# Kernel optimization log

Hardware: AMD Instinct MI355X
Metric: run time of the kernel (lower is better)

Reference implementation:

```python
import jax, jax.numpy as jnp
import numpy as np
from jax import lax

H = 1024   # hidden_size
C = 64     # cond_size
L = 256    # latent_size
V = 32000  # num_of_word
NC = 8     # num_of_cond
T = 256    # MAX_LENGTH == seq len (teacher forcing, full length)


def setup_inputs() -> dict:
    key = jax.random.key(0)
    ks = jax.random.split(key, 26)
    p = lambda k, shape, s=0.05: (jax.random.normal(k, shape, jnp.float32) * s)
    inp = {
        # learned parameters
        "cond_emb": p(ks[0], (NC, C)),
        "enc_emb": p(ks[1], (V, H)),
        "enc_wih": p(ks[2], (4 * H, H)), "enc_whh": p(ks[3], (4 * H, H)),
        "enc_bih": p(ks[4], (4 * H,)), "enc_bhh": p(ks[5], (4 * H,)),
        "mean_w": p(ks[6], (L, H)), "mean_b": p(ks[7], (L,)),
        "lgv_w": p(ks[8], (L, H)), "lgv_b": p(ks[9], (L,)),
        "l2h_w": p(ks[10], (H, L + C)), "l2h_b": p(ks[11], (H,)),
        "l2c_w": p(ks[12], (H, L + C)), "l2c_b": p(ks[13], (H,)),
        "dec_emb": p(ks[14], (V, H)),
        "dec_wih": p(ks[15], (4 * H, H)), "dec_whh": p(ks[16], (4 * H, H)),
        "dec_bih": p(ks[17], (4 * H,)), "dec_bhh": p(ks[18], (4 * H,)),
        "out_w": p(ks[19], (V, H)), "out_b": p(ks[20], (V,)),
        # reparameterization noise (torch.normal in sample_z)
        "eps": jax.random.normal(ks[21], (L,), jnp.float32),
        # forward args
        "input_ids": jax.random.randint(ks[22], (T,), 0, V),
        "target_ids": jax.random.randint(ks[23], (T,), 0, V),
        "input_c": 2,
        "target_c": 3,
    }
    return inp


def _lstm_cell(h, c, x, wih, whh, bih, bhh):
    # torch LSTM gate order: i, f, g, o
    g = x @ wih.T + bih + h @ whh.T + bhh
    i, f, gg, o = jnp.split(g, 4)
    c = jax.nn.sigmoid(f) * c + jax.nn.sigmoid(i) * jnp.tanh(gg)
    h = jax.nn.sigmoid(o) * jnp.tanh(c)
    return h, c


def reference(cond_emb, enc_emb, enc_wih, enc_whh, enc_bih, enc_bhh,
              mean_w, mean_b, lgv_w, lgv_b, l2h_w, l2h_b, l2c_w, l2c_b,
              dec_emb, dec_wih, dec_whh, dec_bih, dec_bhh, out_w, out_b,
              eps, input_ids, target_ids, input_c, target_c):
    Hd = enc_whh.shape[1]
    cond_in = cond_emb[input_c]                              # (C,)
    # encoder initial hidden = cat(zeros(H-C), cond); cell = zeros(H)
    h0 = jnp.concatenate([jnp.zeros(Hd - cond_in.shape[0], cond_in.dtype), cond_in])
    c0 = jnp.zeros(Hd, cond_in.dtype)
    enc_x = enc_emb[input_ids]                               # (T, H)

    def enc_step(carry, x):
        h, c = _lstm_cell(carry[0], carry[1], x, enc_wih, enc_whh, enc_bih, enc_bhh)
        return (h, c), None
    (hT, _), _ = lax.scan(enc_step, (h0, c0), enc_x)

    m = mean_w @ hT + mean_b                                 # (L,)
    lgv = lgv_w @ hT + lgv_b                                 # (L,)
    z = eps * jnp.exp(lgv / 2) + m                           # reparameterize

    zc = jnp.concatenate([z, cond_emb[target_c]])            # (L+C,)
    dh0 = l2h_w @ zc + l2h_b
    dc0 = l2c_w @ zc + l2c_b

    # teacher forcing: decoder inputs = [SOS=0, target[:-1]], T steps
    dec_in = jnp.concatenate([jnp.zeros((1,), target_ids.dtype), target_ids[:-1]])
    dec_x = dec_emb[dec_in]                                  # (T, H)

    def dec_step(carry, x):
        h, c = _lstm_cell(carry[0], carry[1], x, dec_wih, dec_whh, dec_bih, dec_bhh)
        return (h, c), h
    _, hs = lax.scan(dec_step, (dh0, dc0), dec_x)            # (T, H)

    logits = hs @ out_w.T + out_b                            # (T, V)
    return logits, m, lgv
```

## Files before the change

kernel.cpp:

```cpp
#include <hip/hip_runtime.h>
#include <hip/hip_bf16.h>

#define HD   1024
#define G4   4096
#define CND  64
#define LAT  256
#define VOC  32000
#define TT   256
#define ZCN  320
#define NWG  128
#define DEC0 301u

typedef unsigned long long u64;
typedef __attribute__((ext_vector_type(8))) short short8;
typedef __attribute__((ext_vector_type(4))) float f32x4;

__device__ __forceinline__ float sigf(float x) { return 1.0f / (1.0f + expf(-x)); }

__device__ __forceinline__ u64 al64(const u64* p) {
    return __hip_atomic_load((u64*)p, __ATOMIC_RELAXED, __HIP_MEMORY_SCOPE_AGENT);
}
__device__ __forceinline__ void as64(u64* p, u64 v) {
    __hip_atomic_store(p, v, __ATOMIC_RELAXED, __HIP_MEMORY_SCOPE_AGENT);
}
__device__ __forceinline__ u64 packhv(float h, unsigned tag) {
    return ((u64)tag << 32) | (u64)__float_as_uint(h);
}

#define BM  128
#define BN  128
#define BK  32
#define LDT 40

__device__ __forceinline__ void cvt2(float x, ushort& h, ushort& l)
{
    unsigned u = __float_as_uint(x);
    h = (ushort)(u >> 16);
    float hif = __uint_as_float(u & 0xffff0000u);
    l = (ushort)(__float_as_uint(x - hif) >> 16);
}
__device__ __forceinline__ unsigned pk(ushort a, ushort b)
{
    return (unsigned)a | ((unsigned)b << 16);
}

__device__ __forceinline__ void stage16(const float* __restrict__ src,
                                        ushort* __restrict__ dh,
                                        ushort* __restrict__ dl)
{
    ushort h[16], l[16];
    #pragma unroll
    for (int i = 0; i < 16; i += 4) {
        float4 v = *(const float4*)(src + i);
        cvt2(v.x, h[i],   l[i]);
        cvt2(v.y, h[i+1], l[i+1]);
        cvt2(v.z, h[i+2], l[i+2]);
        cvt2(v.w, h[i+3], l[i+3]);
    }
    uint4 H0 = {pk(h[0],h[1]), pk(h[2],h[3]), pk(h[4],h[5]), pk(h[6],h[7])};
    uint4 H1 = {pk(h[8],h[9]), pk(h[10],h[11]), pk(h[12],h[13]), pk(h[14],h[15])};
    uint4 L0 = {pk(l[0],l[1]), pk(l[2],l[3]), pk(l[4],l[5]), pk(l[6],l[7])};
    uint4 L1 = {pk(l[8],l[9]), pk(l[10],l[11]), pk(l[12],l[13]), pk(l[14],l[15])};
    *(uint4*)(dh)     = H0;
    *(uint4*)(dh + 8) = H1;
    *(uint4*)(dl)     = L0;
    *(uint4*)(dl + 8) = L1;
}

__global__ __launch_bounds__(256) void k_gemm3(
    const float* __restrict__ A, const int* __restrict__ ids, int shift,
    const float* __restrict__ B, const float* __restrict__ bias1,
    const float* __restrict__ bias2, float* __restrict__ C,
    int ntn, int ldc)
{
    __shared__ ushort Ah[BM * LDT], Al[BM * LDT];
    __shared__ ushort Bh[BM * LDT], Bl[BM * LDT];

    const int bid  = blockIdx.x;
    const int m0   = (bid / ntn) * BM;
    const int n0   = (bid % ntn) * BN;
    const int tid  = threadIdx.x;
    const int lane = tid & 63;
    const int wid  = tid >> 6;
    const int wm   = (wid >> 1) * 64;
    const int wn   = (wid & 1) * 64;

    const int sr = tid >> 1;
    const int sc = (tid & 1) * 16;

    int ar = m0 + sr;
    if (ids) ar = shift ? ((ar == 0) ? 0 : ids[ar - 1]) : ids[ar];
    const float* arow = A + (size_t)ar * HD;
    const float* brow = B + (size_t)(n0 + sr) * HD;

    f32x4 acc[4][4] = {};

    const int fr = lane & 15;
    const int kg = (lane >> 4) * 8;

    for (int k0 = 0; k0 < HD; k0 += BK) {
        __syncthreads();
        stage16(arow + k0 + sc, &Ah[sr * LDT + sc], &Al[sr * LDT + sc]);
        stage16(brow + k0 + sc, &Bh[sr * LDT + sc], &Bl[sr * LDT + sc]);
        __syncthreads();

        short8 fah[4], fal[4], fbh[4], fbl[4];
        #pragma unroll
        for (int f = 0; f < 4; ++f) {
            fah[f] = *(const short8*)&Ah[(wm + f * 16 + fr) * LDT + kg];
            fal[f] = *(const short8*)&Al[(wm + f * 16 + fr) * LDT + kg];
            fbh[f] = *(const short8*)&Bh[(wn + f * 16 + fr) * LDT + kg];
            fbl[f] = *(const short8*)&Bl[(wn + f * 16 + fr) * LDT + kg];
        }
        #pragma unroll
        for (int fi = 0; fi < 4; ++fi)
            #pragma unroll
            for (int fj = 0; fj < 4; ++fj) {
                acc[fi][fj] = __builtin_amdgcn_mfma_f32_16x16x32_bf16(
                                  fah[fi], fbh[fj], acc[fi][fj], 0, 0, 0);
                acc[fi][fj] = __builtin_amdgcn_mfma_f32_16x16x32_bf16(
                                  fah[fi], fbl[fj], acc[fi][fj], 0, 0, 0);
                acc[fi][fj] = __builtin_amdgcn_mfma_f32_16x16x32_bf16(
                                  fal[fi], fbh[fj], acc[fi][fj], 0, 0, 0);
            }
    }

    const int rg = (lane >> 4) * 4;
    #pragma unroll
    for (int fj = 0; fj < 4; ++fj) {
        int col = n0 + wn + fj * 16 + fr;
        float bs = bias1[col];
        if (bias2) bs += bias2[col];
        #pragma unroll
        for (int fi = 0; fi < 4; ++fi) {
            #pragma unroll
            for (int r = 0; r < 4; ++r) {
                int rowi = m0 + wm + fi * 16 + rg + r;
                C[(size_t)rowi * ldc + col] = acc[fi][fj][r] + bs;
            }
        }
    }
}

#define WCH 132

__device__ __forceinline__ void load_w(float4 (&wreg)[32],
                                       const float* __restrict__ w,
                                       int row, int s)
{
    const float4* p = (const float4*)(w + (size_t)row * HD + s * 128);
    #pragma unroll
    for (int u = 0; u < 32; ++u) wreg[u] = p[u];
}

__device__ __forceinline__ void read_h(const u64* mb, unsigned v,
                                       float* h_lds, int tid)
{
    const u64* p = mb + (size_t)(v & 1u) * HD + tid * 4;
    u64 e0, e1, e2, e3;
    for (;;) {
        e0 = al64(p); e1 = al64(p + 1); e2 = al64(p + 2); e3 = al64(p + 3);
        if ((unsigned)(e0 >> 32) >= v && (unsigned)(e1 >> 32) >= v &&
            (unsigned)(e2 >> 32) >= v && (unsigned)(e3 >> 32) >= v) break;
        __builtin_amdgcn_s_sleep(1);
    }
    float4 hv = make_float4(__uint_as_float((unsigned)e0),
                            __uint_as_float((unsigned)e1),
                            __uint_as_float((unsigned)e2),
                            __uint_as_float((unsigned)e3));
    *(float4*)&h_lds[(tid >> 5) * WCH + (tid & 31) * 4] = hv;
}

__device__ __forceinline__ void lstm_loop(
    const float* __restrict__ pre, u64* mb, float* __restrict__ hs,
    float& c_reg, const float4 (&wreg)[32], float* h_lds, float* g_lds,
    int tid, int s, int rl, int row, int j_own, unsigned vbase)
{
    for (int t = 0; t < TT; ++t) {
        unsigned v = vbase + (unsigned)t;
        float pv = 0.f;
        if (s == 0) pv = pre[(size_t)t * G4 + row];

        read_h(mb, v, h_lds, tid);
        __syncthreads();

        const float4* h4 = (const float4*)h_lds;
        float a0 = 0.f, a1 = 0.f, a2 = 0.f, a3 = 0.f;
        #pragma unroll
        for (int u = 0; u < 32; ++u) {
            float4 wv = wreg[u];
            float4 hv = h4[s * 33 + u];
            a0 = fmaf(wv.x, hv.x, a0);
            a1 = fmaf(wv.y, hv.y, a1);
            a2 = fmaf(wv.z, hv.z, a2);
            a3 = fmaf(wv.w, hv.w, a3);
        }
        float acc = (a0 + a1) + (a2 + a3);
        acc += __shfl_xor(acc, 1);
        acc += __shfl_xor(acc, 2);
        acc += __shfl_xor(acc, 4);
        if (s == 0) g_lds[rl] = acc + pv;
        __syncthreads();

        if (tid < 8) {
            float xi = g_lds[tid],      xf = g_lds[8 + tid];
            float xg = g_lds[16 + tid], xo = g_lds[24 + tid];
            c_reg = sigf(xf) * c_reg + sigf(xi) * tanhf(xg);
            float hv = sigf(xo) * tanhf(c_reg);
            as64(&mb[(size_t)((v + 1u) & 1u) * HD + j_own], packhv(hv, v + 1u));
            if (hs) hs[(size_t)t * HD + j_own] = hv;
        }
    }
}

__global__ __launch_bounds__(256, 1) void k_seq(
    const float* __restrict__ cond_emb, const float* __restrict__ enc_whh,
    const float* __restrict__ mean_w, const float* __restrict__ mean_b,
    const float* __restrict__ lgv_w, const float* __restrict__ lgv_b,
    const float* __restrict__ l2h_w, const float* __restrict__ l2h_b,
    const float* __restrict__ l2c_w, const float* __restrict__ l2c_b,
    const float* __restrict__ dec_whh, const float* __restrict__ eps,
    const int* __restrict__ p_ic, const int* __restrict__ p_tc,
    const float* __restrict__ pre_enc, const float* __restrict__ pre_dec,
    u64* mb, u64* zmb,
    float* __restrict__ hs, float* __restrict__ out_mlgv)
{
    __shared__ float h_lds[8 * WCH];
    __shared__ float g_lds[32];
    __shared__ float red[16];
    __shared__ float sm[4];

    const int w   = blockIdx.x;
    const int tid = threadIdx.x;
    const int s   = tid & 7;
    const int rl  = tid >> 3;
    const int gate = rl >> 3;
    const int jl   = rl & 7;
    const int row  = gate * HD + w * 8 + jl;
    const int j_own = w * 8 + tid;
    float c_reg = 0.f;

    if (tid < 8) {
        int j = j_own;
        float v0 = 0.f;
        int ic = p_ic[0];
        if (j >= HD - CND) v0 = cond_emb[ic * CND + (j - (HD - CND))];
        as64(&mb[(size_t)1 * HD + j], packhv(v0, 1u));
    }

    float4 wreg[32];
    load_w(wreg, enc_whh, row, s);
    lstm_loop(pre_enc, mb, nullptr, c_reg, wreg, h_lds, g_lds,
              tid, s, rl, row, j_own, 1u);

    read_h(mb, TT + 1u, h_lds, tid);
    __syncthreads();
    {
        int d = tid >> 6;
        int l64 = tid & 63;
        int l = w * 2 + (d & 1);
        const float* wrow = (d < 2 ? mean_w : lgv_w) + (size_t)l * HD;
        float acc = 0.f;
        #pragma unroll
        for (int e = 0; e < 16; ++e) {
            int k = e * 64 + l64;
            acc = fmaf(wrow[k], h_lds[(k >> 7) * WCH + (k & 127)], acc);
        }
        #pragma unroll
        for (int o = 32; o >= 1; o >>= 1) acc += __shfl_xor(acc, o);
        if (l64 == 0) sm[d] = acc + (d < 2 ? mean_b : lgv_b)[l];
    }
    __syncthreads();
    if (tid < 2) {
        int l = w * 2 + tid;
        float m = sm[tid], lg = sm[2 + tid];
        float z = eps[l] * expf(0.5f * lg) + m;
        as64(&zmb[l], packhv(z, 1u));
        out_mlgv[l]       = m;
        out_mlgv[LAT + l] = lg;
    }

    {
        u64 e;
        const u64* p = zmb + tid;
        do { e = al64(p); } while ((unsigned)(e >> 32) < 1u);
        h_lds[tid] = __uint_as_float((unsigned)e);
    }
    if (tid < CND) {
        int tc = p_tc[0];
        h_lds[LAT + tid] = cond_emb[tc * CND + tid];
    }
    __syncthreads();
    {
        int r2 = tid >> 4;
        int l16 = tid & 15;
        int which = r2 >> 3;
        int i = w * 8 + (r2 & 7);
        const float* wrow = (which ? l2c_w : l2h_w) + (size_t)i * ZCN;
        float acc = 0.f;
        #pragma unroll
        for (int e = 0; e < 20; ++e) {
            int k = e * 16 + l16;
            acc = fmaf(wrow[k], h_lds[k], acc);
        }
        acc += __shfl_xor(acc, 1);
        acc += __shfl_xor(acc, 2);
        acc += __shfl_xor(acc, 4);
        acc += __shfl_xor(acc, 8);
        if (l16 == 0) red[r2] = acc + (which ? l2c_b : l2h_b)[i];
    }
    __syncthreads();
    if (tid < 8) {
        as64(&mb[(size_t)(DEC0 & 1u) * HD + j_own], packhv(red[tid], DEC0));
        c_reg = red[8 + tid];
    }

    load_w(wreg, dec_whh, row, s);
    lstm_loop(pre_dec, mb, hs, c_reg, wreg, h_lds, g_lds,
              tid, s, rl, row, j_own, DEC0);
}

extern "C" void kernel_launch(void* const* d_in, const int* in_sizes, int n_in,
                              void* d_out, int out_size, void* d_ws, size_t ws_size,
                              hipStream_t stream)
{
    const float* cond_emb = (const float*)d_in[0];
    const float* enc_emb  = (const float*)d_in[1];
    const float* enc_wih  = (const float*)d_in[2];
    const float* enc_whh  = (const float*)d_in[3];
    const float* enc_bih  = (const float*)d_in[4];
    const float* enc_bhh  = (const float*)d_in[5];
    const float* mean_w   = (const float*)d_in[6];
    const float* mean_b   = (const float*)d_in[7];
    const float* lgv_w    = (const float*)d_in[8];
    const float* lgv_b    = (const float*)d_in[9];
    const float* l2h_w    = (const float*)d_in[10];
    const float* l2h_b    = (const float*)d_in[11];
    const float* l2c_w    = (const float*)d_in[12];
    const float* l2c_b    = (const float*)d_in[13];
    const float* dec_emb  = (const float*)d_in[14];
    const float* dec_wih  = (const float*)d_in[15];
    const float* dec_whh  = (const float*)d_in[16];
    const float* dec_bih  = (const float*)d_in[17];
    const float* dec_bhh  = (const float*)d_in[18];
    const float* out_w    = (const float*)d_in[19];
    const float* out_b    = (const float*)d_in[20];
    const float* eps      = (const float*)d_in[21];
    const int* input_ids  = (const int*)d_in[22];
    const int* target_ids = (const int*)d_in[23];
    const int* p_ic       = (const int*)d_in[24];
    const int* p_tc       = (const int*)d_in[25];

    float* ws      = (float*)d_ws;
    float* pre_enc = ws;
    float* pre_dec = pre_enc + (size_t)TT * G4;
    float* hs      = pre_dec + (size_t)TT * G4;
    u64*   mb      = (u64*)(hs + (size_t)TT * HD);
    u64*   zmb     = mb + 2 * HD;

    float* outp     = (float*)d_out;
    float* out_mlgv = outp + (size_t)TT * VOC;

    const int* no_ids = nullptr;
    const float* no_bias = nullptr;

    hipMemsetAsync(mb, 0, (2 * HD + LAT) * sizeof(u64), stream);

    {
        void* a0[] = {(void*)&enc_emb, (void*)&input_ids, (void*)&(int&)*(new int(0)),
                      (void*)&enc_wih, (void*)&enc_bih, (void*)&enc_bhh,
                      (void*)&pre_enc, (void*)&(int&)*(new int(32)), (void*)&(int&)*(new int(G4))};
        (void)a0;
    }
    int shift0 = 0, shift1 = 1, ntn_pre = 32, ldc_pre = G4, ntn_out = 250, ldc_out = VOC;
    (void)shift0;

    hipLaunchKernelGGL(k_gemm3, dim3(2 * 32), dim3(256), 0, stream,
                       enc_emb, input_ids, 0, enc_wih, enc_bih, enc_bhh,
                       pre_enc, ntn_pre, ldc_pre);
    hipLaunchKernelGGL(k_gemm3, dim3(2 * 32), dim3(256), 0, stream,
                       dec_emb, target_ids, shift1, dec_wih, dec_bih, dec_bhh,
                       pre_dec, ntn_pre, ldc_pre);

    void* args[] = {
        (void*)&cond_emb, (void*)&enc_whh, (void*)&mean_w, (void*)&mean_b,
        (void*)&lgv_w, (void*)&lgv_b, (void*)&l2h_w, (void*)&l2h_b,
        (void*)&l2c_w, (void*)&l2c_b, (void*)&dec_whh, (void*)&eps,
        (void*)&p_ic, (void*)&p_tc, (void*)&pre_enc, (void*)&pre_dec,
        (void*)&mb, (void*)&zmb, (void*)&hs, (void*)&out_mlgv
    };
    hipLaunchCooperativeKernel((const void*)k_seq, dim3(NWG), dim3(256),
                               args, 0, stream);

    hipLaunchKernelGGL(k_gemm3, dim3(2 * 250), dim3(256), 0, stream,
                       hs, no_ids, 0, out_w, out_b, no_bias,
                       outp, ntn_out, ldc_out);
}
```

Measured before the change: 1.370 ms.

## Halve recurrent workgroups to 64 with 512 threads, parallelize gate activations

The cooperative LSTM recurrence kernel now runs on 64 workgroups of 512 threads, each owning 16 hidden units instead of 8. This halves the number of groups polling the shared hidden-state mailbox each step. Gate nonlinearities are now computed in parallel across 64 lanes and combined with shuffles, using fast __expf-based sigmoid and tanh. The input-projection value for the next step is prefetched a step ahead. Fewer, larger groups cut cross-CU synchronization fan-in, at the cost of fewer CUs and two waves per SIMD competing for the register-resident weights; the fast math slightly changes numerics.

```diff
diff --git a/kernel.cpp b/kernel.cpp
--- a/kernel.cpp
+++ b/kernel.cpp
@@ -8,14 +8,21 @@
 #define VOC  32000
 #define TT   256
 #define ZCN  320
-#define NWG  128
+#define NWG  64
+#define THR  512
 #define DEC0 301u
 
 typedef unsigned long long u64;
 typedef __attribute__((ext_vector_type(8))) short short8;
 typedef __attribute__((ext_vector_type(4))) float f32x4;
 
-__device__ __forceinline__ float sigf(float x) { return 1.0f / (1.0f + expf(-x)); }
+__device__ __forceinline__ float sig_f(float x) {
+    return 1.0f / (1.0f + __expf(-x));
+}
+__device__ __forceinline__ float tanh_f(float x) {
+    float e = __expf(2.0f * x);
+    return 1.0f - 2.0f / (e + 1.0f);
+}
 
 __device__ __forceinline__ u64 al64(const u64* p) {
     return __hip_atomic_load((u64*)p, __ATOMIC_RELAXED, __HIP_MEMORY_SCOPE_AGENT);
@@ -156,19 +163,17 @@
 __device__ __forceinline__ void read_h(const u64* mb, unsigned v,
                                        float* h_lds, int tid)
 {
-    const u64* p = mb + (size_t)(v & 1u) * HD + tid * 4;
-    u64 e0, e1, e2, e3;
+    const u64* p = mb + (size_t)(v & 1u) * HD + tid * 2;
+    u64 e0, e1;
     for (;;) {
-        e0 = al64(p); e1 = al64(p + 1); e2 = al64(p + 2); e3 = al64(p + 3);
-        if ((unsigned)(e0 >> 32) >= v && (unsigned)(e1 >> 32) >= v &&
-            (unsigned)(e2 >> 32) >= v && (unsigned)(e3 >> 32) >= v) break;
+        e0 = al64(p); e1 = al64(p + 1);
+        if ((unsigned)(e0 >> 32) >= v && (unsigned)(e1 >> 32) >= v) break;
         __builtin_amdgcn_s_sleep(1);
     }
-    float4 hv = make_float4(__uint_as_float((unsigned)e0),
-                            __uint_as_float((unsigned)e1),
-                            __uint_as_float((unsigned)e2),
-                            __uint_as_float((unsigned)e3));
-    *(float4*)&h_lds[(tid >> 5) * WCH + (tid & 31) * 4] = hv;
+    int j = tid * 2;
+    *(float2*)&h_lds[(j >> 7) * WCH + (j & 127)] =
+        make_float2(__uint_as_float((unsigned)e0),
+                    __uint_as_float((unsigned)e1));
 }
 
 __device__ __forceinline__ void lstm_loop(
@@ -176,10 +181,11 @@
     float& c_reg, const float4 (&wreg)[32], float* h_lds, float* g_lds,
     int tid, int s, int rl, int row, int j_own, unsigned vbase)
 {
+    float pv = (s == 0) ? pre[row] : 0.f;
     for (int t = 0; t < TT; ++t) {
         unsigned v = vbase + (unsigned)t;
-        float pv = 0.f;
-        if (s == 0) pv = pre[(size_t)t * G4 + row];
+        float pv_nxt = 0.f;
+        if (s == 0 && t + 1 < TT) pv_nxt = pre[(size_t)(t + 1) * G4 + row];
 
         read_h(mb, v, h_lds, tid);
         __syncthreads();
@@ -202,18 +208,25 @@
         if (s == 0) g_lds[rl] = acc + pv;
         __syncthreads();
 
-        if (tid < 8) {
-            float xi = g_lds[tid],      xf = g_lds[8 + tid];
-            float xg = g_lds[16 + tid], xo = g_lds[24 + tid];
-            c_reg = sigf(xf) * c_reg + sigf(xi) * tanhf(xg);
-            float hv = sigf(xo) * tanhf(c_reg);
-            as64(&mb[(size_t)((v + 1u) & 1u) * HD + j_own], packhv(hv, v + 1u));
-            if (hs) hs[(size_t)t * HD + j_own] = hv;
-        }
-    }
-}
-
-__global__ __launch_bounds__(256, 1) void k_seq(
+        if (tid < 64) {
+            float g = g_lds[tid];
+            float a = (tid >= 32 && tid < 48) ? tanh_f(g) : sig_f(g);
+            float xf = __shfl(a, tid + 16);
+            float xg = __shfl(a, tid + 32);
+            float xo = __shfl(a, tid + 48);
+            if (tid < 16) {
+                c_reg = xf * c_reg + a * xg;
+                float hv = xo * tanh_f(c_reg);
+                as64(&mb[(size_t)((v + 1u) & 1u) * HD + j_own],
+                     packhv(hv, v + 1u));
+                if (hs) hs[(size_t)t * HD + j_own] = hv;
+            }
+        }
+        pv = pv_nxt;
+    }
+}
+
+__global__ __launch_bounds__(512, 1) void k_seq(
     const float* __restrict__ cond_emb, const float* __restrict__ enc_whh,
     const float* __restrict__ mean_w, const float* __restrict__ mean_b,
     const float* __restrict__ lgv_w, const float* __restrict__ lgv_b,
@@ -226,21 +239,21 @@
     float* __restrict__ hs, float* __restrict__ out_mlgv)
 {
     __shared__ float h_lds[8 * WCH];
-    __shared__ float g_lds[32];
-    __shared__ float red[16];
-    __shared__ float sm[4];
+    __shared__ float g_lds[64];
+    __shared__ float red[32];
+    __shared__ float sm[8];
 
     const int w   = blockIdx.x;
     const int tid = threadIdx.x;
     const int s   = tid & 7;
     const int rl  = tid >> 3;
-    const int gate = rl >> 3;
-    const int jl   = rl & 7;
-    const int row  = gate * HD + w * 8 + jl;
-    const int j_own = w * 8 + tid;
+    const int gate = rl >> 4;
+    const int jl   = rl & 15;
+    const int row  = gate * HD + w * 16 + jl;
+    const int j_own = w * 16 + tid;
     float c_reg = 0.f;
 
-    if (tid < 8) {
+    if (tid < 16) {
         int j = j_own;
         float v0 = 0.f;
         int ic = p_ic[0];
@@ -258,8 +271,8 @@
     {
         int d = tid >> 6;
         int l64 = tid & 63;
-        int l = w * 2 + (d & 1);
-        const float* wrow = (d < 2 ? mean_w : lgv_w) + (size_t)l * HD;
+        int l = w * 4 + (d & 3);
+        const float* wrow = (d < 4 ? mean_w : lgv_w) + (size_t)l * HD;
         float acc = 0.f;
         #pragma unroll
         for (int e = 0; e < 16; ++e) {
@@ -268,34 +281,33 @@
         }
         #pragma unroll
         for (int o = 32; o >= 1; o >>= 1) acc += __shfl_xor(acc, o);
-        if (l64 == 0) sm[d] = acc + (d < 2 ? mean_b : lgv_b)[l];
+        if (l64 == 0) sm[d] = acc + (d < 4 ? mean_b : lgv_b)[l];
     }
     __syncthreads();
-    if (tid < 2) {
-        int l = w * 2 + tid;
-        float m = sm[tid], lg = sm[2 + tid];
-        float z = eps[l] * expf(0.5f * lg) + m;
+    if (tid < 4) {
+        int l = w * 4 + tid;
+        float m = sm[tid], lg = sm[4 + tid];
+        float z = eps[l] * __expf(0.5f * lg) + m;
         as64(&zmb[l], packhv(z, 1u));
         out_mlgv[l]       = m;
         out_mlgv[LAT + l] = lg;
     }
 
-    {
+    if (tid < LAT) {
         u64 e;
         const u64* p = zmb + tid;
         do { e = al64(p); } while ((unsigned)(e >> 32) < 1u);
         h_lds[tid] = __uint_as_float((unsigned)e);
-    }
-    if (tid < CND) {
+    } else if (tid < ZCN) {
         int tc = p_tc[0];
-        h_lds[LAT + tid] = cond_emb[tc * CND + tid];
+        h_lds[tid] = cond_emb[tc * CND + (tid - LAT)];
     }
     __syncthreads();
     {
         int r2 = tid >> 4;
         int l16 = tid & 15;
-        int which = r2 >> 3;
-        int i = w * 8 + (r2 & 7);
+        int which = r2 >> 4;
+        int i = w * 16 + (r2 & 15);
         const float* wrow = (which ? l2c_w : l2h_w) + (size_t)i * ZCN;
         float acc = 0.f;
         #pragma unroll
@@ -310,9 +322,9 @@
         if (l16 == 0) red[r2] = acc + (which ? l2c_b : l2h_b)[i];
     }
     __syncthreads();
-    if (tid < 8) {
+    if (tid < 16) {
         as64(&mb[(size_t)(DEC0 & 1u) * HD + j_own], packhv(red[tid], DEC0));
-        c_reg = red[8 + tid];
+        c_reg = red[16 + tid];
     }
 
     load_w(wreg, dec_whh, row, s);
@@ -366,21 +378,12 @@
 
     hipMemsetAsync(mb, 0, (2 * HD + LAT) * sizeof(u64), stream);
 
-    {
-        void* a0[] = {(void*)&enc_emb, (void*)&input_ids, (void*)&(int&)*(new int(0)),
-                      (void*)&enc_wih, (void*)&enc_bih, (void*)&enc_bhh,
-                      (void*)&pre_enc, (void*)&(int&)*(new int(32)), (void*)&(int&)*(new int(G4))};
-        (void)a0;
-    }
-    int shift0 = 0, shift1 = 1, ntn_pre = 32, ldc_pre = G4, ntn_out = 250, ldc_out = VOC;
-    (void)shift0;
-
     hipLaunchKernelGGL(k_gemm3, dim3(2 * 32), dim3(256), 0, stream,
                        enc_emb, input_ids, 0, enc_wih, enc_bih, enc_bhh,
-                       pre_enc, ntn_pre, ldc_pre);
+                       pre_enc, 32, G4);
     hipLaunchKernelGGL(k_gemm3, dim3(2 * 32), dim3(256), 0, stream,
-                       dec_emb, target_ids, shift1, dec_wih, dec_bih, dec_bhh,
-                       pre_dec, ntn_pre, ldc_pre);
+                       dec_emb, target_ids, 1, dec_wih, dec_bih, dec_bhh,
+                       pre_dec, 32, G4);
 
     void* args[] = {
         (void*)&cond_emb, (void*)&enc_whh, (void*)&mean_w, (void*)&mean_b,
@@ -389,10 +392,10 @@
         (void*)&p_ic, (void*)&p_tc, (void*)&pre_enc, (void*)&pre_dec,
         (void*)&mb, (void*)&zmb, (void*)&hs, (void*)&out_mlgv
     };
-    hipLaunchCooperativeKernel((const void*)k_seq, dim3(NWG), dim3(256),
+    hipLaunchCooperativeKernel((const void*)k_seq, dim3(NWG), dim3(THR),
                                args, 0, stream);
 
     hipLaunchKernelGGL(k_gemm3, dim3(2 * 250), dim3(256), 0, stream,
                        hs, no_ids, 0, out_w, out_b, no_bias,
-                       outp, ntn_out, ldc_out);
-}
+                       outp, 250, VOC);
+}
```

New measurement: 1.216 ms. 1.13x faster.
